# Kernel tuning notes

Hardware: AMD Instinct MI355X
Metric: run time of the kernel (lower is better)

Reference implementation:

```python
import jax, jax.numpy as jnp
import numpy as np

E, TOPK, C = 8, 2, 1  # num_local_experts, num_experts_per_tok, num_channels
BS, L, D, F = 8, 1024, 1024, 4096


def setup_inputs() -> dict:
    key = jax.random.key(0)
    ks = jax.random.split(key, 5)
    s = lambda fan_in: 1.0 / np.sqrt(fan_in)
    return {
        "hidden_states": jax.random.normal(ks[0], (BS, L, D), jnp.float32),
        # nn.Linear weight layout [out, in]
        "router_w": jax.random.normal(ks[1], (E, D * C), jnp.float32) * s(D * C),
        "w1": jax.random.normal(ks[2], (E, F, D), jnp.float32) * s(D),
        "w2": jax.random.normal(ks[3], (E, D, F), jnp.float32) * s(F),
        "w3": jax.random.normal(ks[4], (E, F, D), jnp.float32) * s(D),
    }


def _forward(hidden_states, router_w, w1, w2, w3):
    bs, seq, d = hidden_states.shape  # 3D path -> c = 1
    c = C
    h = hidden_states.reshape(bs, seq, c * d)  # [bs, L, c*d]
    # router: per-position logits, then mean over sequence (sentence-level routing)
    router_logits = jnp.einsum('blf,ef->ble', h, router_w).mean(axis=1)  # [bs, E]
    router_probs = jax.nn.softmax(router_logits, axis=-1)
    topk_w, topk_idx = jax.lax.top_k(router_probs, TOPK)  # [bs, TOPK]

    # dense all-expert SwiGLU MLP on every token (as in the original)
    x = h.reshape(bs, seq, c, d)
    outs = []
    for e in range(E):  # fixed small expert count
        up = jnp.einsum('blcd,fd->blcf', x, w1[e])
        gate = jnp.einsum('blcd,fd->blcf', x, w3[e])
        y = jnp.einsum('blcf,df->blcd', jax.nn.silu(up) * gate, w2[e])
        outs.append(y.reshape(bs, seq, c * d))
    expert_outputs = jnp.stack(outs, axis=1)  # [bs, E, L, c*d]

    # Faithful replication of torch.gather(dim=1) with index [bs,L,TOPK,h]:
    # out[b,l,j,:] = expert_outputs[b, topk_idx[b,j], j, :]  (independent of l)
    bi = jnp.arange(bs)[:, None]
    ji = jnp.arange(TOPK)[None, :]
    sel = expert_outputs[bi, topk_idx, ji]  # [bs, TOPK, c*d]
    combined = (sel * topk_w[..., None]).sum(axis=1)  # [bs, c*d]
    out = jnp.broadcast_to(combined[:, None, :], (bs, seq, c * d))
    out = out.reshape(bs, c, seq, d)
    return out, router_logits


def reference(hidden_states, router_w, w1, w2, w3):
    return _forward(hidden_states, router_w, w1, w2, w3)
```

## Files before the change

### kernel.cpp

```cpp
#include <hip/hip_runtime.h>
#include <math.h>

#define BS 8
#define SEQ 1024
#define DIM 1024
#define FF 4096
#define NE 8
#define TOPK 2
#define NSLOT (BS*TOPK)
#define MAXM 8
#define NCHUNK 64
#define UG_TILE 32
#define DN_TILE 16

#define WS_PARTIAL 0
#define WS_LOGITS  (WS_PARTIAL + BS*NCHUNK*DIM)
#define WS_SELW    (WS_LOGITS + BS*NE)
#define WS_SELE    (WS_SELW + NSLOT)
#define WS_ACT     (WS_SELE + NSLOT)
#define WS_Y       (WS_ACT + NSLOT*FF)

__device__ __forceinline__ float dot4(float4 a, float4 b) {
    return a.x*b.x + a.y*b.y + a.z*b.z + a.w*b.w;
}

__global__ __launch_bounds__(256) void kmean(const float4* __restrict__ h4,
                                             float4* __restrict__ part4) {
    const int c = blockIdx.x, b = blockIdx.y, t = threadIdx.x;
    const int LPER = SEQ / NCHUNK;
    const float4* p = h4 + ((size_t)b * SEQ + (size_t)c * LPER) * (DIM/4) + t;
    float4 a = make_float4(0.f, 0.f, 0.f, 0.f);
    #pragma unroll
    for (int i = 0; i < LPER; ++i) {
        float4 v = p[(size_t)i * (DIM/4)];
        a.x += v.x; a.y += v.y; a.z += v.z; a.w += v.w;
    }
    part4[((size_t)(b * NCHUNK + c)) * (DIM/4) + t] = a;
}

__global__ __launch_bounds__(256) void krouter(const float4* __restrict__ part4,
                                               const float4* __restrict__ rw4,
                                               float* __restrict__ out_logits,
                                               float* __restrict__ selw,
                                               int* __restrict__ sele) {
    const int b = blockIdx.x, t = threadIdx.x;
    const float4* p = part4 + (size_t)b * NCHUNK * (DIM/4) + t;
    float4 s = make_float4(0.f, 0.f, 0.f, 0.f);
    #pragma unroll 4
    for (int c = 0; c < NCHUNK; ++c) {
        float4 v = p[(size_t)c * (DIM/4)];
        s.x += v.x; s.y += v.y; s.z += v.z; s.w += v.w;
    }
    const float inv = 1.0f / (float)SEQ;
    s.x *= inv; s.y *= inv; s.z *= inv; s.w *= inv;

    __shared__ float red[4];
    __shared__ float lg[NE];
    const int wave = t >> 6, lane = t & 63;
    for (int e = 0; e < NE; ++e) {
        float4 w = rw4[(size_t)e * (DIM/4) + t];
        float pd = dot4(s, w);
        #pragma unroll
        for (int o = 32; o; o >>= 1) pd += __shfl_xor(pd, o);
        if (lane == 0) red[wave] = pd;
        __syncthreads();
        if (t == 0) {
            float l = red[0] + red[1] + red[2] + red[3];
            lg[e] = l;
            out_logits[b * NE + e] = l;
        }
        __syncthreads();
    }
    if (t == 0) {
        float l[NE];
        float mx = -1e30f;
        #pragma unroll
        for (int e = 0; e < NE; ++e) { l[e] = lg[e]; mx = fmaxf(mx, l[e]); }
        float sum = 0.f;
        #pragma unroll
        for (int e = 0; e < NE; ++e) { l[e] = expf(l[e] - mx); sum += l[e]; }
        const float invs = 1.f / sum;
        float v1 = -1.f, v2 = -1.f; int e1 = -1, e2 = -1;
        #pragma unroll
        for (int e = 0; e < NE; ++e) {
            float pe = l[e] * invs;
            if (pe > v1)      { v2 = v1; e2 = e1; v1 = pe; e1 = e; }
            else if (pe > v2) { v2 = pe; e2 = e; }
        }
        selw[b * 2 + 0] = v1; sele[b * 2 + 0] = e1;
        selw[b * 2 + 1] = v2; sele[b * 2 + 1] = e2;
    }
}

__device__ __forceinline__ int build_slots(const int* __restrict__ sele, int e, int* slot) {
    unsigned mask = 0;
    #pragma unroll
    for (int s = 0; s < NSLOT; ++s) mask |= (sele[s] == e) ? (1u << s) : 0u;
    const int m = __popc(mask);
    unsigned mm = mask;
    #pragma unroll
    for (int ti = 0; ti < MAXM; ++ti) { slot[ti] = __ffs(mm) - 1; mm &= mm - 1; }
    return m;
}

template<int M>
__device__ __forceinline__ void upgate_work(const float4* __restrict__ h4,
                                            const float4* __restrict__ w1_4,
                                            const float4* __restrict__ w3_4,
                                            float* __restrict__ act,
                                            const int* slot, int e, int tile, int t) {
    const int wave = t >> 6, g = (t >> 4) & 3, l = t & 15;
    const float4* xp[M];
    #pragma unroll
    for (int ti = 0; ti < M; ++ti) {
        const int s = slot[ti];
        xp[ti] = h4 + ((size_t)((s >> 1) * SEQ + (s & 1))) * (DIM/4) + l;
    }
    #pragma unroll
    for (int k = 0; k < 2; ++k) {
        const int row = tile * UG_TILE + wave * 8 + k * 4 + g;
        const float4* w1r = w1_4 + ((size_t)e * FF + row) * (DIM/4) + l;
        const float4* w3r = w3_4 + ((size_t)e * FF + row) * (DIM/4) + l;
        float up[M], gt[M];
        #pragma unroll
        for (int ti = 0; ti < M; ++ti) { up[ti] = 0.f; gt[ti] = 0.f; }
        #pragma unroll
        for (int it = 0; it < 16; ++it) {
            float4 a = w1r[it * 16];
            float4 c = w3r[it * 16];
            #pragma unroll
            for (int ti = 0; ti < M; ++ti) {
                float4 x = xp[ti][it * 16];
                up[ti] += dot4(a, x);
                gt[ti] += dot4(c, x);
            }
        }
        #pragma unroll
        for (int ti = 0; ti < M; ++ti) {
            float u = up[ti], gg = gt[ti];
            #pragma unroll
            for (int o = 8; o; o >>= 1) { u += __shfl_xor(u, o); gg += __shfl_xor(gg, o); }
            if (l == 0) {
                act[(size_t)slot[ti] * FF + row] = (u / (1.f + expf(-u))) * gg;
            }
        }
    }
}

__global__ __launch_bounds__(256) void kupgate(const float4* __restrict__ h4,
                                               const float4* __restrict__ w1_4,
                                               const float4* __restrict__ w3_4,
                                               const int* __restrict__ sele,
                                               float* __restrict__ act) {
    const int e = blockIdx.y, tile = blockIdx.x, t = threadIdx.x;
    int slot[MAXM];
    const int m = build_slots(sele, e, slot);
    if (m == 0) return;
    switch (m) {
        case 1: upgate_work<1>(h4, w1_4, w3_4, act, slot, e, tile, t); break;
        case 2: upgate_work<2>(h4, w1_4, w3_4, act, slot, e, tile, t); break;
        case 3: upgate_work<3>(h4, w1_4, w3_4, act, slot, e, tile, t); break;
        case 4: upgate_work<4>(h4, w1_4, w3_4, act, slot, e, tile, t); break;
        case 5: upgate_work<5>(h4, w1_4, w3_4, act, slot, e, tile, t); break;
        case 6: upgate_work<6>(h4, w1_4, w3_4, act, slot, e, tile, t); break;
        case 7: upgate_work<7>(h4, w1_4, w3_4, act, slot, e, tile, t); break;
        default: upgate_work<8>(h4, w1_4, w3_4, act, slot, e, tile, t); break;
    }
}

template<int M>
__device__ __forceinline__ void down_work(const float4* __restrict__ w2_4,
                                          const float4* __restrict__ act4,
                                          const float* __restrict__ selw,
                                          float* __restrict__ y,
                                          const int* slot, int e, int tile, int t) {
    const int wave = t >> 6, g = (t >> 4) & 3, l = t & 15;
    const float4* ap[M];
    float sw[M];
    #pragma unroll
    for (int ti = 0; ti < M; ++ti) {
        ap[ti] = act4 + (size_t)slot[ti] * (FF/4) + l;
        sw[ti] = selw[slot[ti]];
    }
    const int row = tile * DN_TILE + wave * 4 + g;
    const float4* w2r = w2_4 + ((size_t)e * DIM + row) * (FF/4) + l;
    float acc[M];
    #pragma unroll
    for (int ti = 0; ti < M; ++ti) acc[ti] = 0.f;
    #pragma unroll 16
    for (int it = 0; it < 64; ++it) {
        float4 w = w2r[it * 16];
        #pragma unroll
        for (int ti = 0; ti < M; ++ti) {
            acc[ti] += dot4(w, ap[ti][it * 16]);
        }
    }
    #pragma unroll
    for (int ti = 0; ti < M; ++ti) {
        float v = acc[ti];
        #pragma unroll
        for (int o = 8; o; o >>= 1) v += __shfl_xor(v, o);
        if (l == 0) y[(size_t)slot[ti] * DIM + row] = sw[ti] * v;
    }
}

__global__ __launch_bounds__(256) void kdown(const float4* __restrict__ w2_4,
                                             const float4* __restrict__ act4,
                                             const int* __restrict__ sele,
                                             const float* __restrict__ selw,
                                             float* __restrict__ y) {
    const int e = blockIdx.y, tile = blockIdx.x, t = threadIdx.x;
    int slot[MAXM];
    const int m = build_slots(sele, e, slot);
    if (m == 0) return;
    switch (m) {
        case 1: down_work<1>(w2_4, act4, selw, y, slot, e, tile, t); break;
        case 2: down_work<2>(w2_4, act4, selw, y, slot, e, tile, t); break;
        case 3: down_work<3>(w2_4, act4, selw, y, slot, e, tile, t); break;
        case 4: down_work<4>(w2_4, act4, selw, y, slot, e, tile, t); break;
        case 5: down_work<5>(w2_4, act4, selw, y, slot, e, tile, t); break;
        case 6: down_work<6>(w2_4, act4, selw, y, slot, e, tile, t); break;
        case 7: down_work<7>(w2_4, act4, selw, y, slot, e, tile, t); break;
        default: down_work<8>(w2_4, act4, selw, y, slot, e, tile, t); break;
    }
}

__global__ __launch_bounds__(256) void kbcast(const float4* __restrict__ y4,
                                              float4* __restrict__ out4) {
    const int b = blockIdx.y, lg = blockIdx.x, t = threadIdx.x;
    float4 y0 = y4[(size_t)(2 * b) * (DIM/4) + t];
    float4 y1 = y4[(size_t)(2 * b + 1) * (DIM/4) + t];
    float4 c = make_float4(y0.x + y1.x, y0.y + y1.y, y0.z + y1.z, y0.w + y1.w);
    size_t base = ((size_t)b * SEQ + (size_t)lg * 8) * (DIM/4) + t;
    #pragma unroll
    for (int i = 0; i < 8; ++i) out4[base + (size_t)i * (DIM/4)] = c;
}

extern "C" void kernel_launch(void* const* d_in, const int* in_sizes, int n_in,
                              void* d_out, int out_size, void* d_ws, size_t ws_size,
                              hipStream_t stream) {
    const float* h  = (const float*)d_in[0];
    const float* rw = (const float*)d_in[1];
    const float* w1 = (const float*)d_in[2];
    const float* w2 = (const float*)d_in[3];
    const float* w3 = (const float*)d_in[4];
    float* out = (float*)d_out;
    float* ws  = (float*)d_ws;

    float* part   = ws + WS_PARTIAL;
    float* selw   = ws + WS_SELW;
    int*   sele   = (int*)(ws + WS_SELE);
    float* act    = ws + WS_ACT;
    float* y      = ws + WS_Y;
    float* out_logits = out + (size_t)BS * SEQ * DIM;

    kmean  <<<dim3(NCHUNK, BS), 256, 0, stream>>>((const float4*)h, (float4*)part);
    krouter<<<BS, 256, 0, stream>>>((const float4*)part, (const float4*)rw, out_logits, selw, sele);
    kupgate<<<dim3(FF / UG_TILE, NE), 256, 0, stream>>>((const float4*)h, (const float4*)w1,
                                                        (const float4*)w3, sele, act);
    kdown  <<<dim3(DIM / DN_TILE, NE), 256, 0, stream>>>((const float4*)w2, (const float4*)act,
                                                         sele, selw, y);
    kbcast <<<dim3(SEQ / 8, BS), 256, 0, stream>>>((const float4*)y, (float4*)out);
}
```

Before: 134.2 us.

## Stage expert weights into LDS via async double-buffered global_load_lds

Rewrites the up/gate and down expert kernels so that weight rows stream into shared memory through asynchronous global-to-LDS loads. The loads are double-buffered, with explicit vmcnt waits and barriers between stages. Activations and selected tokens are also staged in LDS once per block, and each wave handles a full row with a 64-lane reduction. The goal is to overlap the weight-streaming memory traffic with compute and reuse the token vectors from LDS. In exchange it adds heavy LDS use (up to 96KB per block), which lowers occupancy, plus barrier overhead.

```diff
diff --git a/kernel.cpp b/kernel.cpp
--- a/kernel.cpp
+++ b/kernel.cpp
@@ -6,22 +6,29 @@
 #define DIM 1024
 #define FF 4096
 #define NE 8
-#define TOPK 2
-#define NSLOT (BS*TOPK)
+#define NSLOT 16
 #define MAXM 8
 #define NCHUNK 64
-#define UG_TILE 32
-#define DN_TILE 16
+
+#define UG_ROWS 32
+#define UG_PAIRS 8
+#define DN_ROWS 16
 
 #define WS_PARTIAL 0
-#define WS_LOGITS  (WS_PARTIAL + BS*NCHUNK*DIM)
-#define WS_SELW    (WS_LOGITS + BS*NE)
+#define WS_SELW    (WS_PARTIAL + BS*NCHUNK*DIM)
 #define WS_SELE    (WS_SELW + NSLOT)
 #define WS_ACT     (WS_SELE + NSLOT)
 #define WS_Y       (WS_ACT + NSLOT*FF)
 
 __device__ __forceinline__ float dot4(float4 a, float4 b) {
     return a.x*b.x + a.y*b.y + a.z*b.z + a.w*b.w;
+}
+
+__device__ __forceinline__ void async16(const float* g, float* l) {
+    __builtin_amdgcn_global_load_lds(
+        (const __attribute__((address_space(1))) unsigned int*)g,
+        (__attribute__((address_space(3))) unsigned int*)l,
+        16, 0, 0);
 }
 
 __global__ __launch_bounds__(256) void kmean(const float4* __restrict__ h4,
@@ -104,124 +111,195 @@
 }
 
 template<int M>
-__device__ __forceinline__ void upgate_work(const float4* __restrict__ h4,
-                                            const float4* __restrict__ w1_4,
-                                            const float4* __restrict__ w3_4,
-                                            float* __restrict__ act,
-                                            const int* slot, int e, int tile, int t) {
-    const int wave = t >> 6, g = (t >> 4) & 3, l = t & 15;
-    const float4* xp[M];
-    #pragma unroll
-    for (int ti = 0; ti < M; ++ti) {
-        const int s = slot[ti];
-        xp[ti] = h4 + ((size_t)((s >> 1) * SEQ + (s & 1))) * (DIM/4) + l;
-    }
-    #pragma unroll
-    for (int k = 0; k < 2; ++k) {
-        const int row = tile * UG_TILE + wave * 8 + k * 4 + g;
-        const float4* w1r = w1_4 + ((size_t)e * FF + row) * (DIM/4) + l;
-        const float4* w3r = w3_4 + ((size_t)e * FF + row) * (DIM/4) + l;
+__device__ void upgate_work(const float* __restrict__ h,
+                            const float* __restrict__ w1e,
+                            const float* __restrict__ w3e,
+                            float* __restrict__ act,
+                            const int* slot, int tile, int t,
+                            float* xs, float* wb) {
+    const int wave = t >> 6, lane = t & 63;
+    const int row0 = tile * UG_ROWS;
+
+    {
+        const int ti = t >> 5, j = t & 31;
+        if (ti < M) {
+            const int s = slot[ti];
+            const float4* src = (const float4*)(h + ((size_t)((s >> 1) * SEQ + (s & 1))) * DIM);
+            float4* dst = (float4*)(xs + ti * 1024);
+            #pragma unroll
+            for (int i = 0; i < 8; ++i) dst[j + i * 32] = src[j + i * 32];
+        }
+    }
+    __syncthreads();
+
+    auto stage = [&](int p) {
+        const size_t rbase = (size_t)(row0 + p * 4 + wave) * DIM + lane * 4;
+        const float* g1 = w1e + rbase;
+        const float* g3 = w3e + rbase;
+        float* l1 = wb + (p & 1) * 8192 + wave * 1024;
+        float* l3 = wb + (p & 1) * 8192 + 4096 + wave * 1024;
+        #pragma unroll
+        for (int r = 0; r < 4; ++r) {
+            async16(g1 + r * 256, l1 + r * 256);
+            async16(g3 + r * 256, l3 + r * 256);
+        }
+    };
+
+    stage(0);
+    for (int p = 0; p < UG_PAIRS; ++p) {
+        if (p + 1 < UG_PAIRS) {
+            stage(p + 1);
+            asm volatile("s_waitcnt vmcnt(8)" ::: "memory");
+        } else {
+            asm volatile("s_waitcnt vmcnt(0)" ::: "memory");
+        }
+        __builtin_amdgcn_s_barrier();
+        __builtin_amdgcn_sched_barrier(0);
+
+        const float4* f1p = (const float4*)(wb + (p & 1) * 8192 + wave * 1024);
+        const float4* f3p = (const float4*)(wb + (p & 1) * 8192 + 4096 + wave * 1024);
         float up[M], gt[M];
         #pragma unroll
         for (int ti = 0; ti < M; ++ti) { up[ti] = 0.f; gt[ti] = 0.f; }
         #pragma unroll
-        for (int it = 0; it < 16; ++it) {
-            float4 a = w1r[it * 16];
-            float4 c = w3r[it * 16];
+        for (int c = 0; c < 4; ++c) {
+            float4 f1 = f1p[c * 64 + lane];
+            float4 f3 = f3p[c * 64 + lane];
             #pragma unroll
             for (int ti = 0; ti < M; ++ti) {
-                float4 x = xp[ti][it * 16];
-                up[ti] += dot4(a, x);
-                gt[ti] += dot4(c, x);
+                float4 xf = ((const float4*)(xs + ti * 1024))[c * 64 + lane];
+                up[ti] += dot4(f1, xf);
+                gt[ti] += dot4(f3, xf);
             }
         }
         #pragma unroll
         for (int ti = 0; ti < M; ++ti) {
-            float u = up[ti], gg = gt[ti];
-            #pragma unroll
-            for (int o = 8; o; o >>= 1) { u += __shfl_xor(u, o); gg += __shfl_xor(gg, o); }
-            if (l == 0) {
-                act[(size_t)slot[ti] * FF + row] = (u / (1.f + expf(-u))) * gg;
-            }
-        }
-    }
-}
-
-__global__ __launch_bounds__(256) void kupgate(const float4* __restrict__ h4,
-                                               const float4* __restrict__ w1_4,
-                                               const float4* __restrict__ w3_4,
+            float u = up[ti], g = gt[ti];
+            #pragma unroll
+            for (int o = 32; o; o >>= 1) { u += __shfl_xor(u, o); g += __shfl_xor(g, o); }
+            if (lane == 0)
+                act[(size_t)slot[ti] * FF + row0 + p * 4 + wave] =
+                    (u / (1.f + expf(-u))) * g;
+        }
+        __builtin_amdgcn_sched_barrier(0);
+        __builtin_amdgcn_s_barrier();
+    }
+}
+
+__global__ __launch_bounds__(256) void kupgate(const float* __restrict__ h,
+                                               const float* __restrict__ w1,
+                                               const float* __restrict__ w3,
                                                const int* __restrict__ sele,
                                                float* __restrict__ act) {
+    __shared__ float xs[MAXM * 1024];
+    __shared__ float wb[2 * 8192];
     const int e = blockIdx.y, tile = blockIdx.x, t = threadIdx.x;
     int slot[MAXM];
     const int m = build_slots(sele, e, slot);
     if (m == 0) return;
+    const float* w1e = w1 + (size_t)e * FF * DIM;
+    const float* w3e = w3 + (size_t)e * FF * DIM;
     switch (m) {
-        case 1: upgate_work<1>(h4, w1_4, w3_4, act, slot, e, tile, t); break;
-        case 2: upgate_work<2>(h4, w1_4, w3_4, act, slot, e, tile, t); break;
-        case 3: upgate_work<3>(h4, w1_4, w3_4, act, slot, e, tile, t); break;
-        case 4: upgate_work<4>(h4, w1_4, w3_4, act, slot, e, tile, t); break;
-        case 5: upgate_work<5>(h4, w1_4, w3_4, act, slot, e, tile, t); break;
-        case 6: upgate_work<6>(h4, w1_4, w3_4, act, slot, e, tile, t); break;
-        case 7: upgate_work<7>(h4, w1_4, w3_4, act, slot, e, tile, t); break;
-        default: upgate_work<8>(h4, w1_4, w3_4, act, slot, e, tile, t); break;
+        case 1: upgate_work<1>(h, w1e, w3e, act, slot, tile, t, xs, wb); break;
+        case 2: upgate_work<2>(h, w1e, w3e, act, slot, tile, t, xs, wb); break;
+        case 3: upgate_work<3>(h, w1e, w3e, act, slot, tile, t, xs, wb); break;
+        case 4: upgate_work<4>(h, w1e, w3e, act, slot, tile, t, xs, wb); break;
+        case 5: upgate_work<5>(h, w1e, w3e, act, slot, tile, t, xs, wb); break;
+        case 6: upgate_work<6>(h, w1e, w3e, act, slot, tile, t, xs, wb); break;
+        case 7: upgate_work<7>(h, w1e, w3e, act, slot, tile, t, xs, wb); break;
+        default: upgate_work<8>(h, w1e, w3e, act, slot, tile, t, xs, wb); break;
     }
 }
 
 template<int M>
-__device__ __forceinline__ void down_work(const float4* __restrict__ w2_4,
-                                          const float4* __restrict__ act4,
-                                          const float* __restrict__ selw,
-                                          float* __restrict__ y,
-                                          const int* slot, int e, int tile, int t) {
-    const int wave = t >> 6, g = (t >> 4) & 3, l = t & 15;
-    const float4* ap[M];
-    float sw[M];
-    #pragma unroll
-    for (int ti = 0; ti < M; ++ti) {
-        ap[ti] = act4 + (size_t)slot[ti] * (FF/4) + l;
-        sw[ti] = selw[slot[ti]];
-    }
-    const int row = tile * DN_TILE + wave * 4 + g;
-    const float4* w2r = w2_4 + ((size_t)e * DIM + row) * (FF/4) + l;
-    float acc[M];
-    #pragma unroll
-    for (int ti = 0; ti < M; ++ti) acc[ti] = 0.f;
-    #pragma unroll 16
-    for (int it = 0; it < 64; ++it) {
-        float4 w = w2r[it * 16];
+__device__ void down_work(const float* __restrict__ w2e,
+                          const float* __restrict__ act,
+                          const float* __restrict__ selw,
+                          float* __restrict__ y,
+                          const int* slot, int tile, int t,
+                          float* as, float* wb) {
+    const int wave = t >> 6, lane = t & 63;
+    const int row0 = tile * DN_ROWS;
+
+    float acc[4][M];
+    #pragma unroll
+    for (int p = 0; p < 4; ++p)
+        #pragma unroll
+        for (int ti = 0; ti < M; ++ti) acc[p][ti] = 0.f;
+
+    auto stagew = [&](int kc_, int p_) {
+        const float* g = w2e + (size_t)(row0 + p_ * 4 + wave) * FF + kc_ * 1024 + lane * 4;
+        float* l = wb + (p_ & 1) * 4096 + wave * 1024;
+        #pragma unroll
+        for (int r = 0; r < 4; ++r) async16(g + r * 256, l + r * 256);
+    };
+
+    for (int kc = 0; kc < 4; ++kc) {
         #pragma unroll
         for (int ti = 0; ti < M; ++ti) {
-            acc[ti] += dot4(w, ap[ti][it * 16]);
-        }
-    }
-    #pragma unroll
-    for (int ti = 0; ti < M; ++ti) {
-        float v = acc[ti];
-        #pragma unroll
-        for (int o = 8; o; o >>= 1) v += __shfl_xor(v, o);
-        if (l == 0) y[(size_t)slot[ti] * DIM + row] = sw[ti] * v;
-    }
-}
-
-__global__ __launch_bounds__(256) void kdown(const float4* __restrict__ w2_4,
-                                             const float4* __restrict__ act4,
+            const float* g = act + (size_t)slot[ti] * FF + kc * 1024 + wave * 256 + lane * 4;
+            async16(g, as + ti * 1024 + wave * 256);
+        }
+        stagew(kc, 0);
+        #pragma unroll
+        for (int p = 0; p < 4; ++p) {
+            if (p < 3) {
+                stagew(kc, p + 1);
+                asm volatile("s_waitcnt vmcnt(4)" ::: "memory");
+            } else {
+                asm volatile("s_waitcnt vmcnt(0)" ::: "memory");
+            }
+            __builtin_amdgcn_s_barrier();
+            __builtin_amdgcn_sched_barrier(0);
+
+            const float4* wf4 = (const float4*)(wb + (p & 1) * 4096 + wave * 1024);
+            #pragma unroll
+            for (int c = 0; c < 4; ++c) {
+                float4 wf = wf4[c * 64 + lane];
+                #pragma unroll
+                for (int ti = 0; ti < M; ++ti) {
+                    float4 af = ((const float4*)(as + ti * 1024))[c * 64 + lane];
+                    acc[p][ti] += dot4(wf, af);
+                }
+            }
+            __builtin_amdgcn_sched_barrier(0);
+            __builtin_amdgcn_s_barrier();
+        }
+    }
+
+    #pragma unroll
+    for (int p = 0; p < 4; ++p)
+        #pragma unroll
+        for (int ti = 0; ti < M; ++ti) {
+            float v = acc[p][ti];
+            #pragma unroll
+            for (int o = 32; o; o >>= 1) v += __shfl_xor(v, o);
+            if (lane == 0)
+                y[(size_t)slot[ti] * DIM + row0 + p * 4 + wave] = selw[slot[ti]] * v;
+        }
+}
+
+__global__ __launch_bounds__(256) void kdown(const float* __restrict__ w2,
+                                             const float* __restrict__ act,
                                              const int* __restrict__ sele,
                                              const float* __restrict__ selw,
                                              float* __restrict__ y) {
+    __shared__ float as[MAXM * 1024];
+    __shared__ float wb[2 * 4096];
     const int e = blockIdx.y, tile = blockIdx.x, t = threadIdx.x;
     int slot[MAXM];
     const int m = build_slots(sele, e, slot);
     if (m == 0) return;
+    const float* w2e = w2 + (size_t)e * DIM * FF;
     switch (m) {
-        case 1: down_work<1>(w2_4, act4, selw, y, slot, e, tile, t); break;
-        case 2: down_work<2>(w2_4, act4, selw, y, slot, e, tile, t); break;
-        case 3: down_work<3>(w2_4, act4, selw, y, slot, e, tile, t); break;
-        case 4: down_work<4>(w2_4, act4, selw, y, slot, e, tile, t); break;
-        case 5: down_work<5>(w2_4, act4, selw, y, slot, e, tile, t); break;
-        case 6: down_work<6>(w2_4, act4, selw, y, slot, e, tile, t); break;
-        case 7: down_work<7>(w2_4, act4, selw, y, slot, e, tile, t); break;
-        default: down_work<8>(w2_4, act4, selw, y, slot, e, tile, t); break;
+        case 1: down_work<1>(w2e, act, selw, y, slot, tile, t, as, wb); break;
+        case 2: down_work<2>(w2e, act, selw, y, slot, tile, t, as, wb); break;
+        case 3: down_work<3>(w2e, act, selw, y, slot, tile, t, as, wb); break;
+        case 4: down_work<4>(w2e, act, selw, y, slot, tile, t, as, wb); break;
+        case 5: down_work<5>(w2e, act, selw, y, slot, tile, t, as, wb); break;
+        case 6: down_work<6>(w2e, act, selw, y, slot, tile, t, as, wb); break;
+        case 7: down_work<7>(w2e, act, selw, y, slot, tile, t, as, wb); break;
+        default: down_work<8>(w2e, act, selw, y, slot, tile, t, as, wb); break;
     }
 }
 
@@ -256,9 +334,7 @@
 
     kmean  <<<dim3(NCHUNK, BS), 256, 0, stream>>>((const float4*)h, (float4*)part);
     krouter<<<BS, 256, 0, stream>>>((const float4*)part, (const float4*)rw, out_logits, selw, sele);
-    kupgate<<<dim3(FF / UG_TILE, NE), 256, 0, stream>>>((const float4*)h, (const float4*)w1,
-                                                        (const float4*)w3, sele, act);
-    kdown  <<<dim3(DIM / DN_TILE, NE), 256, 0, stream>>>((const float4*)w2, (const float4*)act,
-                                                         sele, selw, y);
+    kupgate<<<dim3(FF / UG_ROWS, NE), 256, 0, stream>>>(h, w1, w3, sele, act);
+    kdown  <<<dim3(DIM / DN_ROWS, NE), 256, 0, stream>>>(w2, act, sele, selw, y);
     kbcast <<<dim3(SEQ / 8, BS), 256, 0, stream>>>((const float4*)y, (float4*)out);
 }
```

Result: slower. 168.6 us (+25.6%).

## Split-K expert GEMVs with shared-memory activations and fused router partial logits

Applied to the files above, without the earlier changes.

The router stage now computes per-chunk partial logits directly in the mean kernel, and a single small block reduces them and does the softmax and top-k. This removes the separate dense partial-sum buffer and the 8-block router pass. The up/gate and down projections are split along K (2 and 4 ways) with more blocks of 128 threads. Token and activation vectors are staged in shared memory, and the SiLU and gating are applied while loading into the down kernel. Partial sums are combined and scaled by the routing weight in the broadcast kernel, at the cost of extra workspace traffic and larger shared-memory use per block.

```diff
diff --git a/kernel.cpp b/kernel.cpp
--- a/kernel.cpp
+++ b/kernel.cpp
@@ -6,76 +6,63 @@
 #define DIM 1024
 #define FF 4096
 #define NE 8
-#define TOPK 2
-#define NSLOT (BS*TOPK)
+#define NSLOT 16
 #define MAXM 8
 #define NCHUNK 64
-#define UG_TILE 32
-#define DN_TILE 16
-
-#define WS_PARTIAL 0
-#define WS_LOGITS  (WS_PARTIAL + BS*NCHUNK*DIM)
-#define WS_SELW    (WS_LOGITS + BS*NE)
-#define WS_SELE    (WS_SELW + NSLOT)
-#define WS_ACT     (WS_SELE + NSLOT)
-#define WS_Y       (WS_ACT + NSLOT*FF)
+
+#define WS_LPART 0
+#define WS_SELW  (WS_LPART + BS*NCHUNK*NE)
+#define WS_SELE  (WS_SELW + NSLOT)
+#define WS_UPP   (WS_SELE + NSLOT)
+#define WS_GTP   (WS_UPP + 2*NSLOT*FF)
+#define WS_YP    (WS_GTP + 2*NSLOT*FF)
 
 __device__ __forceinline__ float dot4(float4 a, float4 b) {
     return a.x*b.x + a.y*b.y + a.z*b.z + a.w*b.w;
 }
 
-__global__ __launch_bounds__(256) void kmean(const float4* __restrict__ h4,
-                                             float4* __restrict__ part4) {
+__global__ __launch_bounds__(256) void klogit(const float4* __restrict__ h4,
+                                              const float4* __restrict__ rw4,
+                                              float* __restrict__ lpart) {
     const int c = blockIdx.x, b = blockIdx.y, t = threadIdx.x;
-    const int LPER = SEQ / NCHUNK;
-    const float4* p = h4 + ((size_t)b * SEQ + (size_t)c * LPER) * (DIM/4) + t;
-    float4 a = make_float4(0.f, 0.f, 0.f, 0.f);
-    #pragma unroll
-    for (int i = 0; i < LPER; ++i) {
+    const float4* p = h4 + ((size_t)b * SEQ + (size_t)c * 16) * (DIM/4) + t;
+    float4 s = make_float4(0.f, 0.f, 0.f, 0.f);
+    #pragma unroll
+    for (int i = 0; i < 16; ++i) {
         float4 v = p[(size_t)i * (DIM/4)];
-        a.x += v.x; a.y += v.y; a.z += v.z; a.w += v.w;
-    }
-    part4[((size_t)(b * NCHUNK + c)) * (DIM/4) + t] = a;
-}
-
-__global__ __launch_bounds__(256) void krouter(const float4* __restrict__ part4,
-                                               const float4* __restrict__ rw4,
-                                               float* __restrict__ out_logits,
-                                               float* __restrict__ selw,
-                                               int* __restrict__ sele) {
-    const int b = blockIdx.x, t = threadIdx.x;
-    const float4* p = part4 + (size_t)b * NCHUNK * (DIM/4) + t;
-    float4 s = make_float4(0.f, 0.f, 0.f, 0.f);
-    #pragma unroll 4
-    for (int c = 0; c < NCHUNK; ++c) {
-        float4 v = p[(size_t)c * (DIM/4)];
         s.x += v.x; s.y += v.y; s.z += v.z; s.w += v.w;
     }
-    const float inv = 1.0f / (float)SEQ;
-    s.x *= inv; s.y *= inv; s.z *= inv; s.w *= inv;
-
     __shared__ float red[4];
-    __shared__ float lg[NE];
     const int wave = t >> 6, lane = t & 63;
     for (int e = 0; e < NE; ++e) {
-        float4 w = rw4[(size_t)e * (DIM/4) + t];
-        float pd = dot4(s, w);
+        float pd = dot4(s, rw4[(size_t)e * (DIM/4) + t]);
         #pragma unroll
         for (int o = 32; o; o >>= 1) pd += __shfl_xor(pd, o);
         if (lane == 0) red[wave] = pd;
         __syncthreads();
-        if (t == 0) {
-            float l = red[0] + red[1] + red[2] + red[3];
-            lg[e] = l;
-            out_logits[b * NE + e] = l;
-        }
+        if (t == 0) lpart[(size_t)(b * NCHUNK + c) * NE + e] = red[0]+red[1]+red[2]+red[3];
         __syncthreads();
     }
-    if (t == 0) {
-        float l[NE];
-        float mx = -1e30f;
-        #pragma unroll
-        for (int e = 0; e < NE; ++e) { l[e] = lg[e]; mx = fmaxf(mx, l[e]); }
+}
+
+__global__ void krouter2(const float* __restrict__ lpart,
+                         float* __restrict__ out_logits,
+                         float* __restrict__ selw, int* __restrict__ sele) {
+    const int t = threadIdx.x;
+    __shared__ float lg[BS * NE];
+    if (t < BS * NE) {
+        const int b = t >> 3, e = t & 7;
+        float s = 0.f;
+        for (int c = 0; c < NCHUNK; ++c) s += lpart[(size_t)(b * NCHUNK + c) * NE + e];
+        s *= (1.0f / (float)SEQ);
+        lg[b * NE + e] = s;
+        out_logits[b * NE + e] = s;
+    }
+    __syncthreads();
+    if (t < BS) {
+        float l[NE]; float mx = -1e30f;
+        #pragma unroll
+        for (int e = 0; e < NE; ++e) { l[e] = lg[t * NE + e]; mx = fmaxf(mx, l[e]); }
         float sum = 0.f;
         #pragma unroll
         for (int e = 0; e < NE; ++e) { l[e] = expf(l[e] - mx); sum += l[e]; }
@@ -87,8 +74,8 @@
             if (pe > v1)      { v2 = v1; e2 = e1; v1 = pe; e1 = e; }
             else if (pe > v2) { v2 = pe; e2 = e; }
         }
-        selw[b * 2 + 0] = v1; sele[b * 2 + 0] = e1;
-        selw[b * 2 + 1] = v2; sele[b * 2 + 1] = e2;
+        selw[t * 2 + 0] = v1; sele[t * 2 + 0] = e1;
+        selw[t * 2 + 1] = v2; sele[t * 2 + 1] = e2;
     }
 }
 
@@ -104,136 +91,167 @@
 }
 
 template<int M>
-__device__ __forceinline__ void upgate_work(const float4* __restrict__ h4,
-                                            const float4* __restrict__ w1_4,
-                                            const float4* __restrict__ w3_4,
-                                            float* __restrict__ act,
-                                            const int* slot, int e, int tile, int t) {
-    const int wave = t >> 6, g = (t >> 4) & 3, l = t & 15;
-    const float4* xp[M];
-    #pragma unroll
-    for (int ti = 0; ti < M; ++ti) {
-        const int s = slot[ti];
-        xp[ti] = h4 + ((size_t)((s >> 1) * SEQ + (s & 1))) * (DIM/4) + l;
-    }
-    #pragma unroll
-    for (int k = 0; k < 2; ++k) {
-        const int row = tile * UG_TILE + wave * 8 + k * 4 + g;
-        const float4* w1r = w1_4 + ((size_t)e * FF + row) * (DIM/4) + l;
-        const float4* w3r = w3_4 + ((size_t)e * FF + row) * (DIM/4) + l;
-        float up[M], gt[M];
-        #pragma unroll
-        for (int ti = 0; ti < M; ++ti) { up[ti] = 0.f; gt[ti] = 0.f; }
-        #pragma unroll
-        for (int it = 0; it < 16; ++it) {
-            float4 a = w1r[it * 16];
-            float4 c = w3r[it * 16];
+__device__ void ug_body(const float* __restrict__ w1e, const float* __restrict__ w3e,
+                        float* __restrict__ upp, float* __restrict__ gtp,
+                        const int* slot, int tile, int kh, int t, const float* xs) {
+    const int wave = t >> 6, lane = t & 63, g = lane >> 2, l = lane & 3;
+    const int r = tile * 32 + wave * 16 + g;
+    const float4* w1p = (const float4*)w1e + ((size_t)r * (DIM/4) + kh * 128 + l);
+    const float4* w3p = (const float4*)w3e + ((size_t)r * (DIM/4) + kh * 128 + l);
+    const float4* xp = (const float4*)xs;
+    float upa[M], gta[M];
+    #pragma unroll
+    for (int ti = 0; ti < M; ++ti) { upa[ti] = 0.f; gta[ti] = 0.f; }
+    #pragma unroll
+    for (int c = 0; c < 4; ++c) {
+        float4 a[8], bb[8];
+        #pragma unroll
+        for (int i = 0; i < 8; ++i) { a[i] = w1p[c*32 + i*4]; bb[i] = w3p[c*32 + i*4]; }
+        #pragma unroll
+        for (int i = 0; i < 8; ++i) {
             #pragma unroll
             for (int ti = 0; ti < M; ++ti) {
-                float4 x = xp[ti][it * 16];
-                up[ti] += dot4(a, x);
-                gt[ti] += dot4(c, x);
+                float4 x = xp[ti*128 + c*32 + i*4 + l];
+                upa[ti] += dot4(a[i], x);
+                gta[ti] += dot4(bb[i], x);
             }
         }
-        #pragma unroll
-        for (int ti = 0; ti < M; ++ti) {
-            float u = up[ti], gg = gt[ti];
-            #pragma unroll
-            for (int o = 8; o; o >>= 1) { u += __shfl_xor(u, o); gg += __shfl_xor(gg, o); }
-            if (l == 0) {
-                act[(size_t)slot[ti] * FF + row] = (u / (1.f + expf(-u))) * gg;
-            }
-        }
-    }
-}
-
-__global__ __launch_bounds__(256) void kupgate(const float4* __restrict__ h4,
-                                               const float4* __restrict__ w1_4,
-                                               const float4* __restrict__ w3_4,
+    }
+    #pragma unroll
+    for (int ti = 0; ti < M; ++ti) {
+        float u = upa[ti], gg = gta[ti];
+        u += __shfl_xor(u, 1); u += __shfl_xor(u, 2);
+        gg += __shfl_xor(gg, 1); gg += __shfl_xor(gg, 2);
+        if (l == 0) {
+            upp[(size_t)kh * NSLOT * FF + (size_t)slot[ti] * FF + r] = u;
+            gtp[(size_t)kh * NSLOT * FF + (size_t)slot[ti] * FF + r] = gg;
+        }
+    }
+}
+
+__global__ __launch_bounds__(128) void kupgate(const float* __restrict__ h,
+                                               const float* __restrict__ w1,
+                                               const float* __restrict__ w3,
                                                const int* __restrict__ sele,
-                                               float* __restrict__ act) {
-    const int e = blockIdx.y, tile = blockIdx.x, t = threadIdx.x;
+                                               float* __restrict__ upp,
+                                               float* __restrict__ gtp) {
+    __shared__ float xs[MAXM * 512];
+    const int tile = blockIdx.x, e = blockIdx.y, kh = blockIdx.z, t = threadIdx.x;
     int slot[MAXM];
     const int m = build_slots(sele, e, slot);
     if (m == 0) return;
+    for (int ti = 0; ti < m; ++ti) {
+        const int s = slot[ti];
+        ((float4*)xs)[ti * 128 + t] =
+            ((const float4*)(h + ((size_t)((s >> 1) * SEQ + (s & 1))) * DIM + kh * 512))[t];
+    }
+    __syncthreads();
+    const float* w1e = w1 + (size_t)e * FF * DIM;
+    const float* w3e = w3 + (size_t)e * FF * DIM;
     switch (m) {
-        case 1: upgate_work<1>(h4, w1_4, w3_4, act, slot, e, tile, t); break;
-        case 2: upgate_work<2>(h4, w1_4, w3_4, act, slot, e, tile, t); break;
-        case 3: upgate_work<3>(h4, w1_4, w3_4, act, slot, e, tile, t); break;
-        case 4: upgate_work<4>(h4, w1_4, w3_4, act, slot, e, tile, t); break;
-        case 5: upgate_work<5>(h4, w1_4, w3_4, act, slot, e, tile, t); break;
-        case 6: upgate_work<6>(h4, w1_4, w3_4, act, slot, e, tile, t); break;
-        case 7: upgate_work<7>(h4, w1_4, w3_4, act, slot, e, tile, t); break;
-        default: upgate_work<8>(h4, w1_4, w3_4, act, slot, e, tile, t); break;
+        case 1: ug_body<1>(w1e, w3e, upp, gtp, slot, tile, kh, t, xs); break;
+        case 2: ug_body<2>(w1e, w3e, upp, gtp, slot, tile, kh, t, xs); break;
+        case 3: ug_body<3>(w1e, w3e, upp, gtp, slot, tile, kh, t, xs); break;
+        case 4: ug_body<4>(w1e, w3e, upp, gtp, slot, tile, kh, t, xs); break;
+        case 5: ug_body<5>(w1e, w3e, upp, gtp, slot, tile, kh, t, xs); break;
+        case 6: ug_body<6>(w1e, w3e, upp, gtp, slot, tile, kh, t, xs); break;
+        case 7: ug_body<7>(w1e, w3e, upp, gtp, slot, tile, kh, t, xs); break;
+        default: ug_body<8>(w1e, w3e, upp, gtp, slot, tile, kh, t, xs); break;
     }
 }
 
 template<int M>
-__device__ __forceinline__ void down_work(const float4* __restrict__ w2_4,
-                                          const float4* __restrict__ act4,
-                                          const float* __restrict__ selw,
-                                          float* __restrict__ y,
-                                          const int* slot, int e, int tile, int t) {
-    const int wave = t >> 6, g = (t >> 4) & 3, l = t & 15;
-    const float4* ap[M];
-    float sw[M];
-    #pragma unroll
-    for (int ti = 0; ti < M; ++ti) {
-        ap[ti] = act4 + (size_t)slot[ti] * (FF/4) + l;
-        sw[ti] = selw[slot[ti]];
-    }
-    const int row = tile * DN_TILE + wave * 4 + g;
-    const float4* w2r = w2_4 + ((size_t)e * DIM + row) * (FF/4) + l;
+__device__ void dn_body(const float* __restrict__ w2e, const float* __restrict__ as_,
+                        float* __restrict__ yp,
+                        const int* slot, int tile, int kq, int t) {
+    const int wave = t >> 6, lane = t & 63, g = lane >> 2, l = lane & 3;
+    const int r = tile * 32 + wave * 16 + g;
+    const float4* wp = (const float4*)w2e + ((size_t)r * (FF/4) + kq * 256 + l);
+    const float4* ap = (const float4*)as_;
     float acc[M];
     #pragma unroll
     for (int ti = 0; ti < M; ++ti) acc[ti] = 0.f;
-    #pragma unroll 16
-    for (int it = 0; it < 64; ++it) {
-        float4 w = w2r[it * 16];
-        #pragma unroll
-        for (int ti = 0; ti < M; ++ti) {
-            acc[ti] += dot4(w, ap[ti][it * 16]);
+    #pragma unroll
+    for (int c = 0; c < 8; ++c) {
+        float4 a[8];
+        #pragma unroll
+        for (int i = 0; i < 8; ++i) a[i] = wp[c*32 + i*4];
+        #pragma unroll
+        for (int i = 0; i < 8; ++i) {
+            #pragma unroll
+            for (int ti = 0; ti < M; ++ti) {
+                acc[ti] += dot4(a[i], ap[ti*256 + c*32 + i*4 + l]);
+            }
         }
     }
     #pragma unroll
     for (int ti = 0; ti < M; ++ti) {
         float v = acc[ti];
-        #pragma unroll
-        for (int o = 8; o; o >>= 1) v += __shfl_xor(v, o);
-        if (l == 0) y[(size_t)slot[ti] * DIM + row] = sw[ti] * v;
-    }
-}
-
-__global__ __launch_bounds__(256) void kdown(const float4* __restrict__ w2_4,
-                                             const float4* __restrict__ act4,
+        v += __shfl_xor(v, 1); v += __shfl_xor(v, 2);
+        if (l == 0) yp[(size_t)kq * NSLOT * DIM + (size_t)slot[ti] * DIM + r] = v;
+    }
+}
+
+__global__ __launch_bounds__(128) void kdown(const float* __restrict__ w2,
+                                             const float* __restrict__ upp,
+                                             const float* __restrict__ gtp,
                                              const int* __restrict__ sele,
-                                             const float* __restrict__ selw,
-                                             float* __restrict__ y) {
-    const int e = blockIdx.y, tile = blockIdx.x, t = threadIdx.x;
+                                             float* __restrict__ yp) {
+    __shared__ float as_[MAXM * 1024];
+    const int tile = blockIdx.x, e = blockIdx.y, kq = blockIdx.z, t = threadIdx.x;
     int slot[MAXM];
     const int m = build_slots(sele, e, slot);
     if (m == 0) return;
+    const float4* upp4 = (const float4*)upp;
+    const float4* gtp4 = (const float4*)gtp;
+    const int HS = NSLOT * FF / 4;
+    for (int ti = 0; ti < m; ++ti) {
+        const int base = slot[ti] * (FF/4) + kq * 256;
+        #pragma unroll
+        for (int q = 0; q < 2; ++q) {
+            const int idx = t * 2 + q;
+            float4 u0 = upp4[base + idx], u1 = upp4[HS + base + idx];
+            float4 g0 = gtp4[base + idx], g1 = gtp4[HS + base + idx];
+            float4 u = make_float4(u0.x+u1.x, u0.y+u1.y, u0.z+u1.z, u0.w+u1.w);
+            float4 gg = make_float4(g0.x+g1.x, g0.y+g1.y, g0.z+g1.z, g0.w+g1.w);
+            float4 r;
+            r.x = (u.x / (1.f + expf(-u.x))) * gg.x;
+            r.y = (u.y / (1.f + expf(-u.y))) * gg.y;
+            r.z = (u.z / (1.f + expf(-u.z))) * gg.z;
+            r.w = (u.w / (1.f + expf(-u.w))) * gg.w;
+            ((float4*)as_)[ti * 256 + idx] = r;
+        }
+    }
+    __syncthreads();
+    const float* w2e = w2 + (size_t)e * DIM * FF;
     switch (m) {
-        case 1: down_work<1>(w2_4, act4, selw, y, slot, e, tile, t); break;
-        case 2: down_work<2>(w2_4, act4, selw, y, slot, e, tile, t); break;
-        case 3: down_work<3>(w2_4, act4, selw, y, slot, e, tile, t); break;
-        case 4: down_work<4>(w2_4, act4, selw, y, slot, e, tile, t); break;
-        case 5: down_work<5>(w2_4, act4, selw, y, slot, e, tile, t); break;
-        case 6: down_work<6>(w2_4, act4, selw, y, slot, e, tile, t); break;
-        case 7: down_work<7>(w2_4, act4, selw, y, slot, e, tile, t); break;
-        default: down_work<8>(w2_4, act4, selw, y, slot, e, tile, t); break;
-    }
-}
-
-__global__ __launch_bounds__(256) void kbcast(const float4* __restrict__ y4,
+        case 1: dn_body<1>(w2e, as_, yp, slot, tile, kq, t); break;
+        case 2: dn_body<2>(w2e, as_, yp, slot, tile, kq, t); break;
+        case 3: dn_body<3>(w2e, as_, yp, slot, tile, kq, t); break;
+        case 4: dn_body<4>(w2e, as_, yp, slot, tile, kq, t); break;
+        case 5: dn_body<5>(w2e, as_, yp, slot, tile, kq, t); break;
+        case 6: dn_body<6>(w2e, as_, yp, slot, tile, kq, t); break;
+        case 7: dn_body<7>(w2e, as_, yp, slot, tile, kq, t); break;
+        default: dn_body<8>(w2e, as_, yp, slot, tile, kq, t); break;
+    }
+}
+
+__global__ __launch_bounds__(256) void kbcast(const float4* __restrict__ yp4,
+                                              const float* __restrict__ selw,
                                               float4* __restrict__ out4) {
     const int b = blockIdx.y, lg = blockIdx.x, t = threadIdx.x;
-    float4 y0 = y4[(size_t)(2 * b) * (DIM/4) + t];
-    float4 y1 = y4[(size_t)(2 * b + 1) * (DIM/4) + t];
-    float4 c = make_float4(y0.x + y1.x, y0.y + y1.y, y0.z + y1.z, y0.w + y1.w);
+    const float w0 = selw[2*b], w1 = selw[2*b+1];
+    float4 acc = make_float4(0.f, 0.f, 0.f, 0.f);
+    #pragma unroll
+    for (int kq = 0; kq < 4; ++kq) {
+        float4 y0 = yp4[kq * (NSLOT*DIM/4) + (2*b) * (DIM/4) + t];
+        float4 y1 = yp4[kq * (NSLOT*DIM/4) + (2*b+1) * (DIM/4) + t];
+        acc.x += w0*y0.x + w1*y1.x; acc.y += w0*y0.y + w1*y1.y;
+        acc.z += w0*y0.z + w1*y1.z; acc.w += w0*y0.w + w1*y1.w;
+    }
     size_t base = ((size_t)b * SEQ + (size_t)lg * 8) * (DIM/4) + t;
     #pragma unroll
-    for (int i = 0; i < 8; ++i) out4[base + (size_t)i * (DIM/4)] = c;
+    for (int i = 0; i < 8; ++i) out4[base + (size_t)i * (DIM/4)] = acc;
 }
 
 extern "C" void kernel_launch(void* const* d_in, const int* in_sizes, int n_in,
@@ -247,18 +265,17 @@
     float* out = (float*)d_out;
     float* ws  = (float*)d_ws;
 
-    float* part   = ws + WS_PARTIAL;
-    float* selw   = ws + WS_SELW;
-    int*   sele   = (int*)(ws + WS_SELE);
-    float* act    = ws + WS_ACT;
-    float* y      = ws + WS_Y;
+    float* lpart = ws + WS_LPART;
+    float* selw  = ws + WS_SELW;
+    int*   sele  = (int*)(ws + WS_SELE);
+    float* upp   = ws + WS_UPP;
+    float* gtp   = ws + WS_GTP;
+    float* yp    = ws + WS_YP;
     float* out_logits = out + (size_t)BS * SEQ * DIM;
 
-    kmean  <<<dim3(NCHUNK, BS), 256, 0, stream>>>((const float4*)h, (float4*)part);
-    krouter<<<BS, 256, 0, stream>>>((const float4*)part, (const float4*)rw, out_logits, selw, sele);
-    kupgate<<<dim3(FF / UG_TILE, NE), 256, 0, stream>>>((const float4*)h, (const float4*)w1,
-                                                        (const float4*)w3, sele, act);
-    kdown  <<<dim3(DIM / DN_TILE, NE), 256, 0, stream>>>((const float4*)w2, (const float4*)act,
-                                                         sele, selw, y);
-    kbcast <<<dim3(SEQ / 8, BS), 256, 0, stream>>>((const float4*)y, (float4*)out);
-}
+    klogit  <<<dim3(NCHUNK, BS), 256, 0, stream>>>((const float4*)h, (const float4*)rw, lpart);
+    krouter2<<<1, 64, 0, stream>>>(lpart, out_logits, selw, sele);
+    kupgate <<<dim3(FF/32, NE, 2), 128, 0, stream>>>(h, w1, w3, sele, upp, gtp);
+    kdown   <<<dim3(DIM/32, NE, 4), 128, 0, stream>>>(w2, upp, gtp, sele, yp);
+    kbcast  <<<dim3(SEQ/8, BS), 256, 0, stream>>>((const float4*)yp, selw, (float4*)out);
+}
```

After: 222.5 us. +65.8%, slower.
